# Kernel optimization log

Hardware: AMD Instinct MI355X
Metric: run time of the kernel (lower is better)

## Reference

```python
import jax, jax.numpy as jnp
import numpy as np

PATCH = 3  # patch_size=3 -> 3x3 displacement window, kernel_size=1, stride=1, dilation_patch=1

def _corr_level(feat1, feat2, channels):
    # spatial_correlation_sample(feat1, feat2, kernel_size=1, patch_size=3,
    #                            stride=1, padding=0, dilation_patch=1)
    # out[b, pi, pj, y, x] = sum_c feat1[b,c,y,x] * feat2[b,c, y+pi-1, x+pj-1]
    b, c, h, w = feat1.shape
    f2p = jnp.pad(feat2, ((0, 0), (0, 0), (1, 1), (1, 1)))  # zero pad displacements
    planes = []
    for di in range(PATCH):
        for dj in range(PATCH):
            planes.append(jnp.sum(feat1 * f2p[:, :, di:di + h, dj:dj + w], axis=1))
    corr = jnp.stack(planes, axis=1)  # [b, 9, h, w] == view(b, ph*pw, h, w)
    return jax.nn.leaky_relu(corr / channels, negative_slope=0.01)


def setup_inputs() -> dict:
    key = jax.random.key(0)
    chans = [512, 1024, 512, 256, 256, 256]
    sizes = [64, 32, 16, 8, 4, 2]
    B = 16
    ks = jax.random.split(key, 12)
    inp = {}
    for i, (c, s) in enumerate(zip(chans, sizes)):
        inp[f"x_pre{i}"] = jax.random.normal(ks[i], (B, c, s, s), dtype=jnp.float32)
        inp[f"x{i}"] = jax.random.normal(ks[6 + i], (B, c, s, s), dtype=jnp.float32)
    return inp


def reference(x_pre0, x_pre1, x_pre2, x_pre3, x_pre4, x_pre5,
              x0, x1, x2, x3, x4, x5):
    chans = [512, 1024, 512, 256, 256, 256]
    x_pre = [x_pre0, x_pre1, x_pre2, x_pre3, x_pre4, x_pre5]
    x = [x0, x1, x2, x3, x4, x5]
    # zip(x, x_pre): feat1 comes from x (current), feat2 from x_pre (previous)
    return tuple(_corr_level(f1, f2, c) for f1, f2, c in zip(x, x_pre, chans))
```

## Files before the change

### kernel.cpp

```cpp
#include <hip/hip_runtime.h>
#include <stdint.h>


struct Lv {
  const float* f1;
  const float* f2;
  int C, ss;
  int csize;
  uint32_t npix;
  uint32_t blk_end;
  uint32_t out_off;
  float invC;
};
struct P { Lv lv[6]; };

__global__ __launch_bounds__(512, 4) void corr_all(P p, float* __restrict__ out) {
  __shared__ float red[8][9 * 128];

  const uint32_t bid = blockIdx.x;
  int l = 0;
#pragma unroll
  for (int i = 0; i < 5; ++i) l += (bid >= p.lv[i].blk_end) ? 1 : 0;
  const Lv L = p.lv[l];
  const uint32_t tile = bid - (l ? p.lv[l - 1].blk_end : 0u);

  const int w = (int)(threadIdx.x >> 6);
  const int lane = (int)(threadIdx.x & 63u);
  const int ss = L.ss;
  const int S = 1 << ss;
  const int S2 = 1 << (2 * ss);

  uint32_t pix0 = tile * 128u + ((uint32_t)lane << 1);
  if (pix0 >= L.npix) pix0 = L.npix - 2u;
  const uint32_t b = pix0 >> (2 * ss);
  const uint32_t yx = pix0 & (uint32_t)(S2 - 1);
  const int y = (int)(yx >> ss);
  const int x0 = (int)(yx & (uint32_t)(S - 1));

  const size_t pbase = ((size_t)(b * (uint32_t)L.C + (uint32_t)(w * L.csize))) << (2 * ss);
  const float* __restrict__ f1p = L.f1 + pbase + yx;
  const float* __restrict__ f2b = L.f2 + pbase;

  int ro[3];
#pragma unroll
  for (int r = 0; r < 3; ++r) {
    int yy = y + r - 1;
    yy = yy < 0 ? 0 : (yy > S - 1 ? S - 1 : yy);
    ro[r] = yy * S + x0;
  }

  float acc[3][3][2];
#pragma unroll
  for (int r = 0; r < 3; ++r)
#pragma unroll
    for (int d = 0; d < 3; ++d)
#pragma unroll
      for (int e = 0; e < 2; ++e) acc[r][d][e] = 0.f;

  const int n = L.csize;
#pragma unroll 4
  for (int j = 0; j < n; ++j) {
    const float2 a = *(const float2*)f1p;
    const float2 v0 = *(const float2*)(f2b + ro[0]);
    const float2 v1 = *(const float2*)(f2b + ro[1]);
    const float2 v2 = *(const float2*)(f2b + ro[2]);
    f1p += S2;
    f2b += S2;
    const float2 vv[3] = {v0, v1, v2};
#pragma unroll
    for (int r = 0; r < 3; ++r) {
      const float pw = __shfl_up(vv[r].y, 1);
      const float nx = __shfl_down(vv[r].x, 1);
      acc[r][0][0] = fmaf(a.x, pw, acc[r][0][0]);
      acc[r][0][1] = fmaf(a.y, vv[r].x, acc[r][0][1]);
      acc[r][1][0] = fmaf(a.x, vv[r].x, acc[r][1][0]);
      acc[r][1][1] = fmaf(a.y, vv[r].y, acc[r][1][1]);
      acc[r][2][0] = fmaf(a.x, vv[r].y, acc[r][2][0]);
      acc[r][2][1] = fmaf(a.y, nx, acc[r][2][1]);
    }
  }

#pragma unroll
  for (int r = 0; r < 3; ++r)
#pragma unroll
    for (int d = 0; d < 3; ++d) {
      const int t = r * 3 + d;
      *(float2*)&red[w][t * 128 + lane * 2] = make_float2(acc[r][d][0], acc[r][d][1]);
    }

  __syncthreads();

  for (int idx = (int)threadIdx.x; idx < 9 * 128; idx += 512) {
    float s = 0.f;
#pragma unroll
    for (int ww = 0; ww < 8; ++ww) s += red[ww][idx];
    const int t = idx >> 7;
    const int pl = idx & 127;
    const uint32_t px = tile * 128u + (uint32_t)pl;
    if (px < L.npix) {
      const uint32_t bb = px >> (2 * ss);
      const uint32_t pyx = px & (uint32_t)(S2 - 1);
      const int py = (int)(pyx >> ss);
      const int pxx = (int)(pyx & (uint32_t)(S - 1));
      const int di = t / 3 - 1;
      const int dj = t - (t / 3) * 3 - 1;
      const int qy = py + di;
      const int qx = pxx + dj;
      float v = 0.f;
      if ((qy >= 0) & (qy < S) & (qx >= 0) & (qx < S)) {
        v = s * L.invC;
        v = v >= 0.f ? v : 0.01f * v;
      }
      out[(size_t)L.out_off + (((size_t)(bb * 9u + (uint32_t)t)) << (2 * ss)) + pyx] = v;
    }
  }
}

extern "C" void kernel_launch(void* const* d_in, const int* in_sizes, int n_in,
                              void* d_out, int out_size, void* d_ws, size_t ws_size,
                              hipStream_t stream) {
  static const int CH[6] = {512, 1024, 512, 256, 256, 256};
  static const int LG[6] = {6, 5, 4, 3, 2, 1};
  static const int PERM[6] = {1, 0, 2, 3, 4, 5};

  const bool interleaved = (n_in >= 2) && (in_sizes[0] == in_sizes[1]);

  uint32_t ooff[6];
  uint32_t oacc = 0;
  for (int i = 0; i < 6; ++i) {
    ooff[i] = oacc;
    const int S = 1 << LG[i];
    oacc += 9u * 16u * (uint32_t)(S * S);
  }

  P pv;
  uint32_t bend = 0;
  for (int k = 0; k < 6; ++k) {
    const int i = PERM[k];
    const int S = 1 << LG[i];
    const uint32_t npix = 16u * (uint32_t)(S * S);
    const uint32_t tiles = (npix + 127u) / 128u;
    Lv& L = pv.lv[k];
    L.f1 = (const float*)d_in[interleaved ? (2 * i + 1) : (6 + i)];
    L.f2 = (const float*)d_in[interleaved ? (2 * i) : i];
    L.C = CH[i];
    L.ss = LG[i];
    L.csize = CH[i] / 8;
    L.npix = npix;
    bend += tiles;
    L.blk_end = bend;
    L.out_off = ooff[i];
    L.invC = 1.0f / (float)CH[i];
  }

  corr_all<<<bend, 512, 0, stream>>>(pv, (float*)d_out);
}
```

Before: 407.4 us.

## Split channel reduction across blocks with a second finalize kernel

The channel reduction is split into chunks (2 or 4 for the large levels), so more blocks share the work. Each block writes its partial sums to workspace, and a new finalize kernel adds the chunks and applies the border mask, scaling and leaky ReLU. The inner loop is also rewritten as a manually double-buffered load/FMA pipeline, and the launch bounds occupancy hint rises from 4 to 6. The cost is a second kernel launch plus extra global traffic for the partial sums; the code falls back to a single chunk when the workspace is too small. Level ordering (PERM) is also removed.

Result: no change. 399.9 us (-1.8%).

```diff
diff --git a/kernel.cpp b/kernel.cpp
--- a/kernel.cpp
+++ b/kernel.cpp
@@ -5,16 +5,54 @@
 struct Lv {
   const float* f1;
   const float* f2;
-  int C, ss;
-  int csize;
+  float* dst;
+  int C, ss, csize;
+  uint32_t tiles;
   uint32_t npix;
   uint32_t blk_end;
-  uint32_t out_off;
+};
+struct P { Lv lv[6]; };
+
+struct Fv {
+  const float* src;
+  uint32_t end;
+  uint32_t cstride;
+  uint32_t nchunk;
+  int ss;
   float invC;
 };
-struct P { Lv lv[6]; };
-
-__global__ __launch_bounds__(512, 4) void corr_all(P p, float* __restrict__ out) {
+struct PF { Fv f[6]; uint32_t total; };
+
+#define LOADIT(A, R0, R1, R2)                 \
+  do {                                        \
+    (A) = *(const float2*)f1p;                \
+    (R0) = *(const float2*)(f2b + ro0);       \
+    (R1) = *(const float2*)(f2b + ro1);       \
+    (R2) = *(const float2*)(f2b + ro2);       \
+    f1p += S2;                                \
+    f2b += S2;                                \
+  } while (0)
+
+#define FMAROW(A, R, r)                                   \
+  do {                                                    \
+    const float pw = __shfl_up((R).y, 1);                 \
+    const float nx = __shfl_down((R).x, 1);               \
+    acc[r][0][0] = fmaf((A).x, pw, acc[r][0][0]);         \
+    acc[r][0][1] = fmaf((A).y, (R).x, acc[r][0][1]);      \
+    acc[r][1][0] = fmaf((A).x, (R).x, acc[r][1][0]);      \
+    acc[r][1][1] = fmaf((A).y, (R).y, acc[r][1][1]);      \
+    acc[r][2][0] = fmaf((A).x, (R).y, acc[r][2][0]);      \
+    acc[r][2][1] = fmaf((A).y, nx, acc[r][2][1]);         \
+  } while (0)
+
+#define FMAIT(A, R0, R1, R2) \
+  do {                       \
+    FMAROW(A, R0, 0);        \
+    FMAROW(A, R1, 1);        \
+    FMAROW(A, R2, 2);        \
+  } while (0)
+
+__global__ __launch_bounds__(512, 6) void corr_part(P p) {
   __shared__ float red[8][9 * 128];
 
   const uint32_t bid = blockIdx.x;
@@ -22,7 +60,9 @@
 #pragma unroll
   for (int i = 0; i < 5; ++i) l += (bid >= p.lv[i].blk_end) ? 1 : 0;
   const Lv L = p.lv[l];
-  const uint32_t tile = bid - (l ? p.lv[l - 1].blk_end : 0u);
+  const uint32_t local = bid - (l ? p.lv[l - 1].blk_end : 0u);
+  const uint32_t chunk = local / L.tiles;
+  const uint32_t tile = local - chunk * L.tiles;
 
   const int w = (int)(threadIdx.x >> 6);
   const int lane = (int)(threadIdx.x & 63u);
@@ -36,18 +76,21 @@
   const uint32_t yx = pix0 & (uint32_t)(S2 - 1);
   const int y = (int)(yx >> ss);
   const int x0 = (int)(yx & (uint32_t)(S - 1));
-
-  const size_t pbase = ((size_t)(b * (uint32_t)L.C + (uint32_t)(w * L.csize))) << (2 * ss);
+  (void)x0;
+
+  const uint32_t c0 = chunk * (uint32_t)(8 * L.csize) + (uint32_t)(w * L.csize);
+  const size_t pbase = ((size_t)(b * (uint32_t)L.C + c0)) << (2 * ss);
   const float* __restrict__ f1p = L.f1 + pbase + yx;
   const float* __restrict__ f2b = L.f2 + pbase;
 
-  int ro[3];
-#pragma unroll
-  for (int r = 0; r < 3; ++r) {
-    int yy = y + r - 1;
-    yy = yy < 0 ? 0 : (yy > S - 1 ? S - 1 : yy);
-    ro[r] = yy * S + x0;
-  }
+  int yy0 = y - 1;
+  yy0 = yy0 < 0 ? 0 : yy0;
+  int yy2 = y + 1;
+  yy2 = yy2 > S - 1 ? S - 1 : yy2;
+  const int xb = (int)(yx & (uint32_t)(S - 1));
+  const int ro0 = yy0 * S + xb;
+  const int ro1 = y * S + xb;
+  const int ro2 = yy2 * S + xb;
 
   float acc[3][3][2];
 #pragma unroll
@@ -58,27 +101,19 @@
       for (int e = 0; e < 2; ++e) acc[r][d][e] = 0.f;
 
   const int n = L.csize;
-#pragma unroll 4
-  for (int j = 0; j < n; ++j) {
-    const float2 a = *(const float2*)f1p;
-    const float2 v0 = *(const float2*)(f2b + ro[0]);
-    const float2 v1 = *(const float2*)(f2b + ro[1]);
-    const float2 v2 = *(const float2*)(f2b + ro[2]);
-    f1p += S2;
-    f2b += S2;
-    const float2 vv[3] = {v0, v1, v2};
-#pragma unroll
-    for (int r = 0; r < 3; ++r) {
-      const float pw = __shfl_up(vv[r].y, 1);
-      const float nx = __shfl_down(vv[r].x, 1);
-      acc[r][0][0] = fmaf(a.x, pw, acc[r][0][0]);
-      acc[r][0][1] = fmaf(a.y, vv[r].x, acc[r][0][1]);
-      acc[r][1][0] = fmaf(a.x, vv[r].x, acc[r][1][0]);
-      acc[r][1][1] = fmaf(a.y, vv[r].y, acc[r][1][1]);
-      acc[r][2][0] = fmaf(a.x, vv[r].y, acc[r][2][0]);
-      acc[r][2][1] = fmaf(a.y, nx, acc[r][2][1]);
-    }
-  }
+  float2 a0, u0, v0, w0;
+  float2 a1, u1, v1, w1;
+  LOADIT(a0, u0, v0, w0);
+#pragma unroll 1
+  for (int j = 0; j + 2 < n; j += 2) {
+    LOADIT(a1, u1, v1, w1);
+    FMAIT(a0, u0, v0, w0);
+    LOADIT(a0, u0, v0, w0);
+    FMAIT(a1, u1, v1, w1);
+  }
+  LOADIT(a1, u1, v1, w1);
+  FMAIT(a0, u0, v0, w0);
+  FMAIT(a1, u1, v1, w1);
 
 #pragma unroll
   for (int r = 0; r < 3; ++r)
@@ -90,6 +125,7 @@
 
   __syncthreads();
 
+  float* dbase = L.dst + (size_t)chunk * 9u * (size_t)L.npix;
   for (int idx = (int)threadIdx.x; idx < 9 * 128; idx += 512) {
     float s = 0.f;
 #pragma unroll
@@ -100,20 +136,41 @@
     if (px < L.npix) {
       const uint32_t bb = px >> (2 * ss);
       const uint32_t pyx = px & (uint32_t)(S2 - 1);
-      const int py = (int)(pyx >> ss);
-      const int pxx = (int)(pyx & (uint32_t)(S - 1));
-      const int di = t / 3 - 1;
-      const int dj = t - (t / 3) * 3 - 1;
-      const int qy = py + di;
-      const int qx = pxx + dj;
-      float v = 0.f;
-      if ((qy >= 0) & (qy < S) & (qx >= 0) & (qx < S)) {
-        v = s * L.invC;
-        v = v >= 0.f ? v : 0.01f * v;
-      }
-      out[(size_t)L.out_off + (((size_t)(bb * 9u + (uint32_t)t)) << (2 * ss)) + pyx] = v;
+      dbase[(((size_t)(bb * 9u + (uint32_t)t)) << (2 * ss)) + pyx] = s;
     }
   }
+}
+
+__global__ __launch_bounds__(256) void corr_fin(PF p, float* __restrict__ out) {
+  const uint32_t e = blockIdx.x * 256u + threadIdx.x;
+  if (e >= p.total) return;
+  int l = 0;
+#pragma unroll
+  for (int i = 0; i < 5; ++i) l += (e >= p.f[i].end) ? 1 : 0;
+  const Fv F = p.f[l];
+  const int ss = F.ss;
+  const int S = 1 << ss;
+  const int S2 = 1 << (2 * ss);
+  const uint32_t local = e - (F.end - F.cstride);
+  const uint32_t bt = local >> (2 * ss);
+  const uint32_t yx = local & (uint32_t)(S2 - 1);
+  const uint32_t t = bt % 9u;
+  const int y = (int)(yx >> ss);
+  const int x = (int)(yx & (uint32_t)(S - 1));
+  const int di = (int)t / 3 - 1;
+  const int dj = (int)t % 3 - 1;
+  const int qy = y + di;
+  const int qx = x + dj;
+
+  float s = 0.f;
+  for (uint32_t k = 0; k < F.nchunk; ++k) s += F.src[(size_t)k * F.cstride + local];
+
+  float v = 0.f;
+  if ((qy >= 0) & (qy < S) & (qx >= 0) & (qx < S)) {
+    v = s * F.invC;
+    v = v >= 0.f ? v : 0.01f * v;
+  }
+  out[e] = v;
 }
 
 extern "C" void kernel_launch(void* const* d_in, const int* in_sizes, int n_in,
@@ -121,37 +178,55 @@
                               hipStream_t stream) {
   static const int CH[6] = {512, 1024, 512, 256, 256, 256};
   static const int LG[6] = {6, 5, 4, 3, 2, 1};
-  static const int PERM[6] = {1, 0, 2, 3, 4, 5};
+  int NCK[6] = {2, 4, 2, 1, 1, 1};
 
   const bool interleaved = (n_in >= 2) && (in_sizes[0] == in_sizes[1]);
 
-  uint32_t ooff[6];
-  uint32_t oacc = 0;
+  uint32_t npixs[6], ooff[6], oacc = 0;
   for (int i = 0; i < 6; ++i) {
+    npixs[i] = 16u << (2 * LG[i]);
     ooff[i] = oacc;
-    const int S = 1 << LG[i];
-    oacc += 9u * 16u * (uint32_t)(S * S);
-  }
-
-  P pv;
+    oacc += 9u * npixs[i];
+  }
+
+  size_t wneed = 0;
+  for (int i = 0; i < 6; ++i) wneed += (size_t)NCK[i] * 9u * npixs[i];
+  wneed *= sizeof(float);
+  const bool fb = (d_ws == nullptr) || (ws_size < wneed);
+  if (fb)
+    for (int i = 0; i < 6; ++i) NCK[i] = 1;
+
+  P p;
+  PF pf;
+  float* ws = (float*)d_ws;
+  float* out = (float*)d_out;
   uint32_t bend = 0;
-  for (int k = 0; k < 6; ++k) {
-    const int i = PERM[k];
-    const int S = 1 << LG[i];
-    const uint32_t npix = 16u * (uint32_t)(S * S);
-    const uint32_t tiles = (npix + 127u) / 128u;
-    Lv& L = pv.lv[k];
+  size_t woff = 0;
+  for (int i = 0; i < 6; ++i) {
+    const uint32_t tiles = (npixs[i] + 127u) / 128u;
+    Lv& L = p.lv[i];
     L.f1 = (const float*)d_in[interleaved ? (2 * i + 1) : (6 + i)];
     L.f2 = (const float*)d_in[interleaved ? (2 * i) : i];
+    L.dst = fb ? (out + ooff[i]) : (ws + woff);
     L.C = CH[i];
     L.ss = LG[i];
-    L.csize = CH[i] / 8;
-    L.npix = npix;
-    bend += tiles;
+    L.csize = CH[i] / (8 * NCK[i]);
+    L.tiles = tiles;
+    L.npix = npixs[i];
+    bend += tiles * (uint32_t)NCK[i];
     L.blk_end = bend;
-    L.out_off = ooff[i];
-    L.invC = 1.0f / (float)CH[i];
-  }
-
-  corr_all<<<bend, 512, 0, stream>>>(pv, (float*)d_out);
+
+    Fv& F = pf.f[i];
+    F.src = L.dst;
+    F.end = ooff[i] + 9u * npixs[i];
+    F.cstride = 9u * npixs[i];
+    F.nchunk = (uint32_t)NCK[i];
+    F.ss = LG[i];
+    F.invC = 1.0f / (float)CH[i];
+    woff += (size_t)NCK[i] * 9u * npixs[i];
+  }
+  pf.total = oacc;
+
+  corr_part<<<bend, 512, 0, stream>>>(p);
+  corr_fin<<<(oacc + 255u) / 256u, 256, 0, stream>>>(pf, out);
 }
```
